# Kernel optimization log

Measured on AMD Instinct MI355X. Metric: run time of the kernel, lower is better.

## Reference

```python
import jax, jax.numpy as jnp
import numpy as np

D = 1024      # model dim
H = 16        # attention heads
E = 8         # experts
TOP_K = 2
CF = 1.25     # capacity factor
EPS = 1e-5
BAL_COEF = 1e-2
Z_COEF = 1e-3


def layer_norm(x, w, b):
    m = x.mean(-1, keepdims=True)
    var = ((x - m) ** 2).mean(-1, keepdims=True)
    return (x - m) * jax.lax.rsqrt(var + EPS) * w + b


def mha(q, k, v, in_w, in_b, out_w, out_b):
    B, S, d = q.shape
    dh = d // H
    wq, wk, wv = jnp.split(in_w, 3, axis=0)
    bq, bk, bv = jnp.split(in_b, 3)

    def proj(x, w, b):  # [B,S,d] -> [B,H,S,dh]
        return (x @ w.T + b).reshape(B, -1, H, dh).transpose(0, 2, 1, 3)

    qh, kh, vh = proj(q, wq, bq), proj(k, wk, bk), proj(v, wv, bv)
    scale = 1.0 / np.sqrt(dh)
    scores = jnp.einsum('bhqd,bhkd->bhqk', qh, kh) * scale
    attn = jax.nn.softmax(scores, axis=-1)
    o = jnp.einsum('bhqk,bhkd->bhqd', attn, vh).transpose(0, 2, 1, 3).reshape(B, S, d)
    return o @ out_w.T + out_b


def moe(x, router_w, w1, b1, w2, b2):
    B, S, d = x.shape
    t = x.reshape(-1, d)           # [N,d] tokens
    N = t.shape[0]
    C = int(np.ceil(TOP_K * N / E * CF))  # per-expert capacity (static)
    logits = t @ router_w          # [N,E]
    probs = jax.nn.softmax(logits, axis=-1)
    gates, idx = jax.lax.top_k(probs, TOP_K)   # [N,2]
    oh = jax.nn.one_hot(idx, E, dtype=t.dtype) # [N,2,E]
    m0, m1 = oh[:, 0], oh[:, 1]
    # position in expert buffer; first choices take priority over second
    pos0 = jnp.cumsum(m0, axis=0) - 1.0
    pos1 = jnp.cumsum(m1, axis=0) - 1.0 + m0.sum(axis=0, keepdims=True)
    v0 = m0 * (pos0 < C)
    v1 = m1 * (pos1 < C)
    p0 = jax.nn.one_hot(pos0.astype(jnp.int32), C, dtype=t.dtype) * v0[..., None]  # [N,E,C]
    p1 = jax.nn.one_hot(pos1.astype(jnp.int32), C, dtype=t.dtype) * v1[..., None]
    dispatch = p0 + p1
    combine = p0 * gates[:, 0, None, None] + p1 * gates[:, 1, None, None]
    # dispatch -> grouped GEMM -> combine
    xin = jnp.einsum('nec,nd->ecd', dispatch, t)                     # [E,C,d]
    h = jax.nn.gelu(jnp.einsum('ecd,edf->ecf', xin, w1) + b1[:, None, :])
    out_e = jnp.einsum('ecf,efd->ecd', h, w2) + b2[:, None, :]       # [E,C,d]
    y = jnp.einsum('nec,ecd->nd', combine, out_e).reshape(B, S, d)
    # aux losses: load-balance + router z-loss
    f = m0.mean(axis=0)            # fraction routed (top-1)
    P = probs.mean(axis=0)         # mean router prob
    balance = E * jnp.sum(f * P)
    zloss = jnp.mean(jax.nn.logsumexp(logits, axis=-1) ** 2)
    aux = BAL_COEF * balance + Z_COEF * zloss
    return y, aux


def setup_inputs() -> dict:
    key = jax.random.key(0)
    ks = jax.random.split(key, 16)
    s = 0.02
    Dff = 4 * D
    return {
        'q': jax.random.normal(ks[0], (8, 512, D), jnp.float32),
        'k': jax.random.normal(ks[1], (8, 512, D), jnp.float32),
        'v': jax.random.normal(ks[2], (8, 512, D), jnp.float32),
        'in_proj_w': jax.random.normal(ks[3], (3 * D, D), jnp.float32) * s,
        'in_proj_b': jnp.zeros((3 * D,), jnp.float32),
        'out_proj_w': jax.random.normal(ks[4], (D, D), jnp.float32) * s,
        'out_proj_b': jnp.zeros((D,), jnp.float32),
        'ln1_w': jnp.ones((D,), jnp.float32),
        'ln1_b': jnp.zeros((D,), jnp.float32),
        'ln2_w': jnp.ones((D,), jnp.float32),
        'ln2_b': jnp.zeros((D,), jnp.float32),
        'router_w': jax.random.normal(ks[5], (D, E), jnp.float32) * s,
        'w1': jax.random.normal(ks[6], (E, D, Dff), jnp.float32) * s,
        'b1': jnp.zeros((E, Dff), jnp.float32),
        'w2': jax.random.normal(ks[7], (E, Dff, D), jnp.float32) * s,
        'b2': jnp.zeros((E, D), jnp.float32),
    }


def reference(q, k, v, in_proj_w, in_proj_b, out_proj_w, out_proj_b,
              ln1_w, ln1_b, ln2_w, ln2_b, router_w, w1, b1, w2, b2):
    attn = mha(q, k, v, in_proj_w, in_proj_b, out_proj_w, out_proj_b)
    x = layer_norm(q + attn, ln1_w, ln1_b)
    y, aux = moe(x, router_w, w1, b1, w2, b2)
    x = layer_norm(x + y, ln2_w, ln2_b)
    return x, aux
```

## Files before the change

kernel.cpp:

```cpp
#include <hip/hip_runtime.h>
#include <cstdint>
#include <cstddef>

#define KB   8
#define KS   512
#define KD   1024
#define KH   16
#define KDH  64
#define KE   8
#define KDFF 4096
#define KN   4096
#define KCAP 1280
#define KCHB 32
#define KNCH 4

typedef unsigned short u16;
typedef _Float16 f16;
typedef f16   f16x8 __attribute__((ext_vector_type(8)));
typedef float f32x4 __attribute__((ext_vector_type(4)));

#define RSCALE 4096.0f
#define RINV   2.44140625e-4f

__device__ __forceinline__ u16 f2h(float f){
  f16 h = (f16)f;
  return __builtin_bit_cast(u16, h);
}
__device__ __forceinline__ float h2f(u16 u){
  f16 h = __builtin_bit_cast(f16, u);
  return (float)h;
}
__device__ __forceinline__ void split2v(float f, u16 &a, u16 &b){
  f16 h0 = (f16)f;
  float r = (f - (float)h0) * RSCALE;
  a = __builtin_bit_cast(u16, h0);
  b = f2h(r);
}
__device__ __forceinline__ f16x8 ld8h(const u16* p){
  uint4 v = *(const uint4*)p;
  return __builtin_bit_cast(f16x8, v);
}
__device__ __forceinline__ void async16(const u16* g, u16* l){
  __builtin_amdgcn_global_load_lds(
      (const __attribute__((address_space(1))) unsigned int*)(g),
      (__attribute__((address_space(3))) unsigned int*)(l),
      16, 0, 0);
}

struct GArgs {
  const u16 *A0, *A1;
  const u16 *B0, *B1;
  long lda, sA, ldb, sB;
  const float* bias; long biasStride;
  float* outF;
  u16 *o0;
  int K, mode;
  float scale;
};

template<int NP>
__launch_bounds__(256)
__global__ void gemm128(GArgs g){
  __shared__ __align__(16) u16 sm[NP*2*4096];
  const int tid  = threadIdx.x;
  const int lane = tid & 63;
  const int wave = tid >> 6;
  const int quad = lane >> 4;
  const int r    = lane & 15;
  const int wm = (wave & 1) * 64;
  const int wn = (wave >> 1) * 64;
  const int z  = blockIdx.z;
  const long m0 = (long)blockIdx.y * 128;
  const long n0 = (long)blockIdx.x * 128;
  const u16* Ap[NP]; const u16* Bp[NP];
  Ap[0] = g.A0 + (long)z*g.sA; Bp[0] = g.B0 + (long)z*g.sB;
  if (NP == 2){ Ap[1] = g.A1 + (long)z*g.sA; Bp[1] = g.B1 + (long)z*g.sB; }
  const int srow   = tid >> 2;
  const int schunk = (tid & 3) ^ ((tid >> 3) & 3);
  f32x4 acc[4][4] = {};
  f32x4 accr[4][4] = {};
  for (int kt = 0; kt < g.K; kt += 32){
#pragma unroll
    for (int p = 0; p < NP; ++p){
#pragma unroll
      for (int r0 = 0; r0 < 2; ++r0){
        long row = r0*64 + srow;
        async16(Ap[p] + (m0 + row)*g.lda + kt + schunk*8, &sm[p*4096      + r0*2048 + wave*512]);
        async16(Bp[p] + (n0 + row)*g.ldb + kt + schunk*8, &sm[(NP+p)*4096 + r0*2048 + wave*512]);
      }
    }
    __syncthreads();
    f16x8 af[NP][4], bf[NP][4];
#pragma unroll
    for (int i = 0; i < 4; ++i){
      int row = wm + i*16 + r;
      int slot = quad ^ ((row >> 1) & 3);
#pragma unroll
      for (int p = 0; p < NP; ++p)
        af[p][i] = ld8h(&sm[p*4096 + row*32 + slot*8]);
    }
#pragma unroll
    for (int j = 0; j < 4; ++j){
      int row = wn + j*16 + r;
      int slot = quad ^ ((row >> 1) & 3);
#pragma unroll
      for (int p = 0; p < NP; ++p)
        bf[p][j] = ld8h(&sm[(NP+p)*4096 + row*32 + slot*8]);
    }
#pragma unroll
    for (int i = 0; i < 4; ++i)
#pragma unroll
      for (int j = 0; j < 4; ++j){
        acc[i][j] = __builtin_amdgcn_mfma_f32_16x16x32_f16(af[0][i], bf[0][j], acc[i][j], 0, 0, 0);
        if (NP == 2){
          accr[i][j] = __builtin_amdgcn_mfma_f32_16x16x32_f16(af[0][i], bf[1][j], accr[i][j], 0, 0, 0);
          accr[i][j] = __builtin_amdgcn_mfma_f32_16x16x32_f16(af[1][i], bf[0][j], accr[i][j], 0, 0, 0);
        }
      }
    __syncthreads();
  }
#pragma unroll
  for (int i = 0; i < 4; ++i){
#pragma unroll
    for (int rr = 0; rr < 4; ++rr){
      long row = m0 + wm + i*16 + quad*4 + rr;
#pragma unroll
      for (int j = 0; j < 4; ++j){
        long col = n0 + wn + j*16 + r;
        float v = acc[i][j][rr];
        if (NP == 2) v += accr[i][j][rr] * RINV;
        switch (g.mode){
          case 2: {
            g.outF[((long)z*KS + row)*KS + col] = v * g.scale;
            break;
          }
          case 4: {
            v += g.bias[col];
            g.outF[row*KD + col] = v;
            break;
          }
          case 5: {
            v += g.bias[(long)z*g.biasStride + col];
            float u = v + 0.044715f*v*v*v;
            v = 0.5f*v*(1.0f + tanhf(0.7978845608028654f*u));
            g.o0[((long)z*KCAP + row)*KDFF + col] = f2h(v);
            break;
          }
          case 6: {
            v += g.bias[(long)z*g.biasStride + col];
            g.o0[((long)z*KCAP + row)*KD + col] = f2h(v);
            break;
          }
          default: {
            v += g.bias[(long)z*g.biasStride + col];
            long b = row >> 9, s = row & 511;
            long h = col >> 6, d = col & 63;
            long idx = (z < 2) ? (((b*KH + h)*KS + s)*KDH + d)
                               : (((b*KH + h)*KDH + d)*KS + s);
            u16* d0 = g.o0 + (long)z * 2 * ((long)KN*KD);
            u16* d1 = d0 + (long)KN*KD;
            unsigned short x, y; split2v(v, x, y);
            d0[idx] = x; d1[idx] = y;
            break;
          }
        }
      }
    }
  }
}

__launch_bounds__(256)
__global__ void gemm_pv(const u16* __restrict__ Ph, const u16* __restrict__ Pl,
                        const u16* __restrict__ V0, const u16* __restrict__ V1,
                        u16* __restrict__ O0, u16* __restrict__ O1, int chunkBase){
  __shared__ __align__(16) u16 sm[2*4096 + 2*2048];
  const int tid  = threadIdx.x;
  const int lane = tid & 63;
  const int wave = tid >> 6;
  const int quad = lane >> 4;
  const int r    = lane & 15;
  const int wm = (wave & 1) * 64;
  const int wn = (wave >> 1) * 32;
  const int z  = blockIdx.y;
  const long m0 = (long)blockIdx.x * 128;
  const u16* Ap[2] = { Ph + (long)z*KS*KS,  Pl + (long)z*KS*KS };
  const u16* Bp[2] = { V0 + (long)z*KDH*KS, V1 + (long)z*KDH*KS };
  const int srow   = tid >> 2;
  const int schunk = (tid & 3) ^ ((tid >> 3) & 3);
  f32x4 acc[4][2] = {};
  f32x4 accr[4][2] = {};
  for (int kt = 0; kt < KS; kt += 32){
#pragma unroll
    for (int p = 0; p < 2; ++p){
#pragma unroll
      for (int r0 = 0; r0 < 2; ++r0){
        long row = r0*64 + srow;
        async16(Ap[p] + (m0 + row)*KS + kt + schunk*8, &sm[p*4096 + r0*2048 + wave*512]);
      }
      async16(Bp[p] + srow*KS + kt + schunk*8, &sm[8192 + p*2048 + wave*512]);
    }
    __syncthreads();
    f16x8 af[2][4], bf[2][2];
#pragma unroll
    for (int i = 0; i < 4; ++i){
      int row = wm + i*16 + r;
      int slot = quad ^ ((row >> 1) & 3);
#pragma unroll
      for (int p = 0; p < 2; ++p)
        af[p][i] = ld8h(&sm[p*4096 + row*32 + slot*8]);
    }
#pragma unroll
    for (int j = 0; j < 2; ++j){
      int row = wn + j*16 + r;
      int slot = quad ^ ((row >> 1) & 3);
#pragma unroll
      for (int p = 0; p < 2; ++p)
        bf[p][j] = ld8h(&sm[8192 + p*2048 + row*32 + slot*8]);
    }
#pragma unroll
    for (int i = 0; i < 4; ++i)
#pragma unroll
      for (int j = 0; j < 2; ++j){
        acc[i][j]  = __builtin_amdgcn_mfma_f32_16x16x32_f16(af[0][i], bf[0][j], acc[i][j], 0, 0, 0);
        accr[i][j] = __builtin_amdgcn_mfma_f32_16x16x32_f16(af[0][i], bf[1][j], accr[i][j], 0, 0, 0);
        accr[i][j] = __builtin_amdgcn_mfma_f32_16x16x32_f16(af[1][i], bf[0][j], accr[i][j], 0, 0, 0);
      }
    __syncthreads();
  }
  int bh = chunkBase + z;
  long b = bh >> 4, h = bh & 15;
#pragma unroll
  for (int i = 0; i < 4; ++i){
#pragma unroll
    for (int rr = 0; rr < 4; ++rr){
      long s = m0 + wm + i*16 + quad*4 + rr;
#pragma unroll
      for (int j = 0; j < 2; ++j){
        long col = wn + j*16 + r;
        float v = acc[i][j][rr] + accr[i][j][rr] * RINV;
        long idx = (b*KS + s)*KD + h*KDH + col;
        unsigned short x, y; split2v(v, x, y);
        O0[idx] = x; O1[idx] = y;
      }
    }
  }
}

__global__ void split2k(const float* __restrict__ x, u16* __restrict__ h,
                        u16* __restrict__ l, long n4){
  long i = (long)blockIdx.x*blockDim.x + threadIdx.x;
  if (i >= n4) return;
  float4 v = ((const float4*)x)[i];
  ushort4 a, b;
  split2v(v.x, a.x, b.x);
  split2v(v.y, a.y, b.y);
  split2v(v.z, a.z, b.z);
  split2v(v.w, a.w, b.w);
  ((ushort4*)h)[i] = a; ((ushort4*)l)[i] = b;
}

__global__ void trans_b(const float* __restrict__ in, u16* __restrict__ outp, int R, int Cc){
  __shared__ float tile[32][33];
  long z = blockIdx.z;
  const float* ip = in + z*(long)R*Cc;
  u16* op = outp + z*(long)R*Cc;
  int c0 = blockIdx.x*32, r0 = blockIdx.y*32;
  int tx = threadIdx.x, ty = threadIdx.y;
  for (int rr = ty; rr < 32; rr += 8)
    tile[rr][tx] = ip[(long)(r0+rr)*Cc + c0 + tx];
  __syncthreads();
  for (int cc = ty; cc < 32; cc += 8)
    op[(long)(c0+cc)*R + r0 + tx] = f2h(tile[tx][cc]);
}

__launch_bounds__(64)
__global__ void softmax2(const float* __restrict__ scores, u16* __restrict__ ph,
                         u16* __restrict__ pl){
  long row = blockIdx.x;
  const float* rp = scores + row * KS;
  int lane = threadIdx.x;
  float4 a = ((const float4*)rp)[lane*2];
  float4 b = ((const float4*)rp)[lane*2 + 1];
  float vv[8] = {a.x,a.y,a.z,a.w,b.x,b.y,b.z,b.w};
  float m = vv[0];
#pragma unroll
  for (int t = 1; t < 8; ++t) m = fmaxf(m, vv[t]);
  for (int off = 32; off; off >>= 1) m = fmaxf(m, __shfl_xor(m, off));
  float s = 0.f;
#pragma unroll
  for (int t = 0; t < 8; ++t){ vv[t] = expf(vv[t] - m); s += vv[t]; }
  for (int off = 32; off; off >>= 1) s += __shfl_xor(s, off);
  float inv = 1.0f / s;
  unsigned short hh[8], ll[8];
#pragma unroll
  for (int t = 0; t < 8; ++t) split2v(vv[t] * inv, hh[t], ll[t]);
  ushort4* dh = (ushort4*)(ph + row*KS + lane*8);
  dh[0] = make_ushort4(hh[0],hh[1],hh[2],hh[3]);
  dh[1] = make_ushort4(hh[4],hh[5],hh[6],hh[7]);
  ushort4* dl = (ushort4*)(pl + row*KS + lane*8);
  dl[0] = make_ushort4(ll[0],ll[1],ll[2],ll[3]);
  dl[1] = make_ushort4(ll[4],ll[5],ll[6],ll[7]);
}

__launch_bounds__(256)
__global__ void ln1_router(const float* __restrict__ q, const float* __restrict__ attn,
    const float* __restrict__ lnw, const float* __restrict__ lnb, const float* __restrict__ rw,
    float* __restrict__ x1, u16* __restrict__ x1b,
    int* __restrict__ idx0, int* __restrict__ idx1, float* __restrict__ gate0, float* __restrict__ gate1,
    float* __restrict__ ptok, float* __restrict__ lset){
  const int t = blockIdx.x, tid = threadIdx.x;
  const int lane = tid & 63, wid = tid >> 6;
  float4 xv = ((const float4*)(q    + (long)t*KD))[tid];
  float4 av = ((const float4*)(attn + (long)t*KD))[tid];
  xv.x += av.x; xv.y += av.y; xv.z += av.z; xv.w += av.w;
  float s  = xv.x + xv.y + xv.z + xv.w;
  float ss = xv.x*xv.x + xv.y*xv.y + xv.z*xv.z + xv.w*xv.w;
  for (int off = 32; off; off >>= 1){ s += __shfl_xor(s, off); ss += __shfl_xor(ss, off); }
  __shared__ float rs[4], rss[4];
  if (lane == 0){ rs[wid] = s; rss[wid] = ss; }
  __syncthreads();
  float S1 = rs[0]+rs[1]+rs[2]+rs[3];
  float S2 = rss[0]+rss[1]+rss[2]+rss[3];
  float mean = S1 * (1.0f/KD);
  float var  = S2 * (1.0f/KD) - mean*mean;
  float rstd = rsqrtf(var + 1e-5f);
  float4 w4 = ((const float4*)lnw)[tid];
  float4 b4 = ((const float4*)lnb)[tid];
  float y0 = (xv.x - mean)*rstd*w4.x + b4.x;
  float y1 = (xv.y - mean)*rstd*w4.y + b4.y;
  float y2 = (xv.z - mean)*rstd*w4.z + b4.z;
  float y3 = (xv.w - mean)*rstd*w4.w + b4.w;
  float4 yo; yo.x=y0; yo.y=y1; yo.z=y2; yo.w=y3;
  ((float4*)(x1 + (long)t*KD))[tid] = yo;
  ushort4 yb; yb.x=f2h(y0); yb.y=f2h(y1); yb.z=f2h(y2); yb.w=f2h(y3);
  ((ushort4*)(x1b + (long)t*KD))[tid] = yb;
  int d0 = tid*4;
  float rloc[4][8];
#pragma unroll
  for (int c = 0; c < 4; ++c){
    const float4* rp = (const float4*)(rw + (long)(d0 + c)*KE);
    float4 u = rp[0], v2 = rp[1];
    rloc[c][0]=u.x; rloc[c][1]=u.y; rloc[c][2]=u.z; rloc[c][3]=u.w;
    rloc[c][4]=v2.x; rloc[c][5]=v2.y; rloc[c][6]=v2.z; rloc[c][7]=v2.w;
  }
  float yv[4] = {y0,y1,y2,y3};
  float pr[8];
#pragma unroll
  for (int e = 0; e < 8; ++e)
    pr[e] = yv[0]*rloc[0][e] + yv[1]*rloc[1][e] + yv[2]*rloc[2][e] + yv[3]*rloc[3][e];
#pragma unroll
  for (int e = 0; e < 8; ++e)
    for (int off = 32; off; off >>= 1) pr[e] += __shfl_xor(pr[e], off);
  __shared__ float wl[4][8];
  if (lane == 0)
#pragma unroll
    for (int e = 0; e < 8; ++e) wl[wid][e] = pr[e];
  __syncthreads();
  if (tid == 0){
    float lg[8];
#pragma unroll
    for (int e = 0; e < 8; ++e) lg[e] = wl[0][e]+wl[1][e]+wl[2][e]+wl[3][e];
    float mx = lg[0];
    for (int e = 1; e < 8; ++e) mx = fmaxf(mx, lg[e]);
    float pe[8], se = 0.f;
    for (int e = 0; e < 8; ++e){ pe[e] = expf(lg[e]-mx); se += pe[e]; }
    float inv = 1.0f/se;
    for (int e = 0; e < 8; ++e) pe[e] *= inv;
    int e0 = 0;
    for (int e = 1; e < 8; ++e) if (pe[e] > pe[e0]) e0 = e;
    int e1 = (e0 == 0) ? 1 : 0;
    for (int e = 0; e < 8; ++e) if (e != e0 && pe[e] > pe[e1]) e1 = e;
    idx0[t] = e0; idx1[t] = e1;
    gate0[t] = pe[e0]; gate1[t] = pe[e1];
    for (int e = 0; e < 8; ++e) ptok[(long)t*8 + e] = pe[e];
    lset[t] = mx + logf(se);
  }
}

__launch_bounds__(64)
__global__ void scan1(const int* __restrict__ idx0, const int* __restrict__ idx1,
                      int* __restrict__ rnk0, int* __restrict__ rnk1,
                      int* __restrict__ h0, int* __restrict__ h1){
  int lane = threadIdx.x;
  int t = blockIdx.x*64 + lane;
  int i0 = idx0[t], i1 = idx1[t];
  unsigned long long below = (1ull << lane) - 1ull;
  unsigned long long b0[8], b1[8];
#pragma unroll
  for (int e = 0; e < 8; ++e){
    b0[e] = __ballot(i0 == e);
    b1[e] = __ballot(i1 == e);
  }
  rnk0[t] = __popcll(b0[i0] & below);
  rnk1[t] = __popcll(b1[i1] & below);
  if (lane < 8){
    h0[blockIdx.x*8 + lane] = __popcll(b0[lane]);
    h1[blockIdx.x*8 + lane] = __popcll(b1[lane]);
  }
}

__launch_bounds__(64)
__global__ void scan2(const int* __restrict__ h0, const int* __restrict__ h1,
                      int* __restrict__ bs0, int* __restrict__ bs1, int* __restrict__ cnt0){
  int lane = threadIdx.x;
  for (int e = 0; e < 8; ++e){
    int v = h0[lane*8 + e];
    int x = v;
    for (int off = 1; off < 64; off <<= 1){
      int y = __shfl_up(x, off);
      if (lane >= off) x += y;
    }
    bs0[lane*8 + e] = x - v;
    int tot = __shfl(x, 63);
    if (lane == 0) cnt0[e] = tot;
    int w = h1[lane*8 + e];
    int xx = w;
    for (int off = 1; off < 64; off <<= 1){
      int y = __shfl_up(xx, off);
      if (lane >= off) xx += y;
    }
    bs1[lane*8 + e] = tot + xx - w;
  }
}

__global__ void scan3(const int* __restrict__ idx0, const int* __restrict__ idx1,
                      const int* __restrict__ rnk0, const int* __restrict__ rnk1,
                      const int* __restrict__ bs0, const int* __restrict__ bs1,
                      int* __restrict__ dst0, int* __restrict__ dst1, int* __restrict__ slot){
  int t = blockIdx.x*blockDim.x + threadIdx.x;
  if (t >= KN) return;
  int c = t >> 6;
  int e0 = idx0[t], e1 = idx1[t];
  int p0 = bs0[c*8 + e0] + rnk0[t];
  int p1 = bs1[c*8 + e1] + rnk1[t];
  int d0 = (p0 < KCAP) ? (e0*KCAP + p0) : -1;
  int d1 = (p1 < KCAP) ? (e1*KCAP + p1) : -1;
  dst0[t] = d0; dst1[t] = d1;
  if (d0 >= 0) slot[d0] = t;
  if (d1 >= 0) slot[d1] = t;
}

__launch_bounds__(64)
__global__ void gather_xin(const int* __restrict__ slot_token, const u16* __restrict__ x1b,
                           u16* __restrict__ xin){
  long slot = blockIdx.x;
  int t = slot_token[slot];
  uint4* dst = (uint4*)(xin + slot*KD);
  int lane = threadIdx.x;
  if (t >= 0){
    const uint4* src = (const uint4*)(x1b + (long)t*KD);
    dst[lane*2]   = src[lane*2];
    dst[lane*2+1] = src[lane*2+1];
  } else {
    uint4 zz; zz.x = zz.y = zz.z = zz.w = 0;
    dst[lane*2] = zz; dst[lane*2+1] = zz;
  }
}

__launch_bounds__(256)
__global__ void combine_ln2(const float* __restrict__ x1, const u16* __restrict__ oute,
    const int* __restrict__ dest0, const int* __restrict__ dest1,
    const float* __restrict__ gate0, const float* __restrict__ gate1,
    const float* __restrict__ lnw, const float* __restrict__ lnb, float* __restrict__ out){
  const int t = blockIdx.x, tid = threadIdx.x;
  const int lane = tid & 63, wid = tid >> 6;
  float4 xv = ((const float4*)(x1 + (long)t*KD))[tid];
  int d0 = dest0[t], d1 = dest1[t];
  float g0 = gate0[t], g1 = gate1[t];
  if (d0 >= 0){
    ushort4 o = ((const ushort4*)(oute + (long)d0*KD))[tid];
    xv.x += g0*h2f(o.x); xv.y += g0*h2f(o.y); xv.z += g0*h2f(o.z); xv.w += g0*h2f(o.w);
  }
  if (d1 >= 0){
    ushort4 o = ((const ushort4*)(oute + (long)d1*KD))[tid];
    xv.x += g1*h2f(o.x); xv.y += g1*h2f(o.y); xv.z += g1*h2f(o.z); xv.w += g1*h2f(o.w);
  }
  float s  = xv.x + xv.y + xv.z + xv.w;
  float ss = xv.x*xv.x + xv.y*xv.y + xv.z*xv.z + xv.w*xv.w;
  for (int off = 32; off; off >>= 1){ s += __shfl_xor(s, off); ss += __shfl_xor(ss, off); }
  __shared__ float rs[4], rss[4];
  if (lane == 0){ rs[wid] = s; rss[wid] = ss; }
  __syncthreads();
  float S1 = rs[0]+rs[1]+rs[2]+rs[3];
  float S2 = rss[0]+rss[1]+rss[2]+rss[3];
  float mean = S1 * (1.0f/KD);
  float var  = S2 * (1.0f/KD) - mean*mean;
  float rstd = rsqrtf(var + 1e-5f);
  float4 w4 = ((const float4*)lnw)[tid];
  float4 b4 = ((const float4*)lnb)[tid];
  float4 yo;
  yo.x = (xv.x - mean)*rstd*w4.x + b4.x;
  yo.y = (xv.y - mean)*rstd*w4.y + b4.y;
  yo.z = (xv.z - mean)*rstd*w4.z + b4.z;
  yo.w = (xv.w - mean)*rstd*w4.w + b4.w;
  ((float4*)(out + (long)t*KD))[tid] = yo;
}

__launch_bounds__(1024)
__global__ void aux_k(const int* __restrict__ cnt0, const float* __restrict__ ptok,
                      const float* __restrict__ lset, float* __restrict__ out){
  int t = threadIdx.x;
  float ps[8] = {0,0,0,0,0,0,0,0};
  float l2 = 0.f;
  for (int i = t; i < KN; i += 1024){
    const float4* p = (const float4*)(ptok + (long)i*8);
    float4 a = p[0], b = p[1];
    ps[0]+=a.x; ps[1]+=a.y; ps[2]+=a.z; ps[3]+=a.w;
    ps[4]+=b.x; ps[5]+=b.y; ps[6]+=b.z; ps[7]+=b.w;
    float l = lset[i]; l2 = fmaf(l, l, l2);
  }
#pragma unroll
  for (int off = 32; off; off >>= 1){
#pragma unroll
    for (int e = 0; e < 8; ++e) ps[e] += __shfl_xor(ps[e], off);
    l2 += __shfl_xor(l2, off);
  }
  __shared__ float sp[16][9];
  int lane = t & 63, wid = t >> 6;
  if (lane == 0){
#pragma unroll
    for (int e = 0; e < 8; ++e) sp[wid][e] = ps[e];
    sp[wid][8] = l2;
  }
  __syncthreads();
  if (t == 0){
    float fin[9];
#pragma unroll
    for (int j = 0; j < 9; ++j){
      float s = 0.f;
      for (int w2 = 0; w2 < 16; ++w2) s += sp[w2][j];
      fin[j] = s;
    }
    float bal = 0.f;
    for (int e = 0; e < 8; ++e)
      bal += ((float)cnt0[e] * (1.0f/KN)) * (fin[e] * (1.0f/KN));
    bal *= (float)KE;
    float zl = fin[8] * (1.0f/KN);
    out[(long)KN*KD] = 0.01f*bal + 0.001f*zl;
  }
}

extern "C" void kernel_launch(void* const* d_in, const int* in_sizes, int n_in,
                              void* d_out, int out_size, void* d_ws, size_t ws_size,
                              hipStream_t stream){
  const float* q    = (const float*)d_in[0];
  const float* k    = (const float*)d_in[1];
  const float* v    = (const float*)d_in[2];
  const float* inw  = (const float*)d_in[3];
  const float* inb  = (const float*)d_in[4];
  const float* outw = (const float*)d_in[5];
  const float* outb = (const float*)d_in[6];
  const float* ln1w = (const float*)d_in[7];
  const float* ln1b = (const float*)d_in[8];
  const float* ln2w = (const float*)d_in[9];
  const float* ln2b = (const float*)d_in[10];
  const float* rw   = (const float*)d_in[11];
  const float* w1   = (const float*)d_in[12];
  const float* b1   = (const float*)d_in[13];
  const float* w2   = (const float*)d_in[14];
  const float* b2   = (const float*)d_in[15];
  float* out = (float*)d_out;
  char* ws = (char*)d_ws;

  constexpr size_t PLB  = (size_t)KN*KD*2;
  constexpr long   PLE  = (long)KN*KD;
  constexpr size_t oW1T = 0;
  constexpr size_t oW2T = oW1T + 67108864;
  constexpr size_t oWQ0 = oW2T + 67108864;
  constexpr size_t oWQ1 = oWQ0 + 6291456;
  constexpr size_t oWO0 = oWQ1 + 6291456;
  constexpr size_t oWO1 = oWO0 + 2097152;
  constexpr size_t oX1  = oWO1 + 2097152;
  constexpr size_t oX1B = oX1  + 16777216;
  constexpr size_t oMISC= oX1B + 8388608;
  constexpr size_t oU1  = oMISC + 1048576;
  constexpr size_t oU2  = oU1 + 83886080;
  constexpr size_t oU3  = oU2 + 50331648;
  constexpr size_t oEND = oU3 + 67108864;
  if (ws_size < oEND) return;

  u16* W1T = (u16*)(ws + oW1T);
  u16* W2T = (u16*)(ws + oW2T);
  u16* WQ0 = (u16*)(ws + oWQ0); u16* WQ1 = (u16*)(ws + oWQ1);
  u16* WO0 = (u16*)(ws + oWO0); u16* WO1 = (u16*)(ws + oWO1);
  float* X1 = (float*)(ws + oX1);
  u16* X1B  = (u16*)(ws + oX1B);

  int*   IDX0 = (int*)(ws + oMISC);
  int*   IDX1 = (int*)(ws + oMISC + 16384);
  int*   RNK0 = (int*)(ws + oMISC + 32768);
  int*   RNK1 = (int*)(ws + oMISC + 49152);
  int*   DST0 = (int*)(ws + oMISC + 65536);
  int*   DST1 = (int*)(ws + oMISC + 81920);
  float* G0   = (float*)(ws + oMISC + 98304);
  float* G1   = (float*)(ws + oMISC + 114688);
  int*   H0   = (int*)(ws + oMISC + 131072);
  int*   H1   = (int*)(ws + oMISC + 133120);
  int*   BS0  = (int*)(ws + oMISC + 135168);
  int*   BS1  = (int*)(ws + oMISC + 137216);
  int*   CNT0 = (int*)(ws + oMISC + 139264);
  int*   SLOT = (int*)(ws + oMISC + 139776);
  float* PTOK = (float*)(ws + oMISC + 262144);
  float* LSET = (float*)(ws + oMISC + 393216);

  u16* Qs0 = (u16*)(ws + oU1);           u16* Qs1 = (u16*)(ws + oU1 + PLB);
  u16* Ks0 = (u16*)(ws + oU1 + 2*PLB);   u16* Ks1 = (u16*)(ws + oU1 + 3*PLB);
  u16* Vs0 = (u16*)(ws + oU1 + 4*PLB);   u16* Vs1 = (u16*)(ws + oU1 + 5*PLB);
  float* ATTN = (float*)(ws + oU1);
  u16* O0 = (u16*)(ws + oU1 + 16777216);
  u16* O1 = (u16*)(ws + oU1 + 16777216 + PLB);
  u16* HBUF = (u16*)(ws + oU1);

  u16* QH0 = (u16*)(ws + oU2);           u16* QH1 = (u16*)(ws + oU2 + PLB);
  u16* KH0 = (u16*)(ws + oU2 + 2*PLB);   u16* KH1 = (u16*)(ws + oU2 + 3*PLB);
  u16* VT0 = (u16*)(ws + oU2 + 4*PLB);   u16* VT1 = (u16*)(ws + oU2 + 5*PLB);
  u16* XIN  = (u16*)(ws + oU2);
  u16* OUTE = (u16*)(ws + oU2 + 20971520);

  float* SCF = (float*)(ws + oU3);
  u16* PH  = (u16*)(ws + oU3 + 33554432);
  u16* PL  = (u16*)(ws + oU3 + 50331648);

  hipMemsetAsync(ws + oMISC + 139776, 0xFF, (size_t)KE*KCAP*4, stream);

  split2k<<<4096, 256, 0, stream>>>(q, Qs0, Qs1, (long)KN*KD/4);
  split2k<<<4096, 256, 0, stream>>>(k, Ks0, Ks1, (long)KN*KD/4);
  split2k<<<4096, 256, 0, stream>>>(v, Vs0, Vs1, (long)KN*KD/4);
  split2k<<<3072, 256, 0, stream>>>(inw, WQ0, WQ1, 786432);
  split2k<<<1024, 256, 0, stream>>>(outw, WO0, WO1, 262144);

  trans_b<<<dim3(KDFF/32, KD/32, KE), dim3(32,8), 0, stream>>>(w1, W1T, KD, KDFF);
  trans_b<<<dim3(KD/32, KDFF/32, KE), dim3(32,8), 0, stream>>>(w2, W2T, KDFF, KD);

  {
    GArgs ga{};
    ga.A0=Qs0; ga.A1=Qs1; ga.lda=KD; ga.sA=2*PLE;
    ga.B0=WQ0; ga.B1=WQ1; ga.ldb=KD; ga.sB=1048576;
    ga.bias=inb; ga.biasStride=KD;
    ga.o0=QH0; ga.outF=nullptr;
    ga.K=KD; ga.mode=7; ga.scale=1.f;
    gemm128<2><<<dim3(8, 32, 3), 256, 0, stream>>>(ga);
  }

  for (int c = 0; c < KNCH; ++c){
    long hoff = (long)c * KCHB * KS * KDH;
    GArgs gs{};
    gs.A0=QH0+hoff; gs.A1=QH1+hoff; gs.lda=KDH; gs.sA=(long)KS*KDH;
    gs.B0=KH0+hoff; gs.B1=KH1+hoff; gs.ldb=KDH; gs.sB=(long)KS*KDH;
    gs.bias=nullptr; gs.biasStride=0; gs.outF=SCF; gs.o0=nullptr;
    gs.K=KDH; gs.mode=2; gs.scale=0.125f;
    gemm128<2><<<dim3(4, 4, KCHB), 256, 0, stream>>>(gs);

    softmax2<<<KCHB*KS, 64, 0, stream>>>(SCF, PH, PL);

    gemm_pv<<<dim3(4, KCHB), 256, 0, stream>>>(PH, PL, VT0+hoff, VT1+hoff,
                                               O0, O1, c*KCHB);
  }

  {
    GArgs go{};
    go.A0=O0; go.A1=O1; go.lda=KD; go.sA=0;
    go.B0=WO0; go.B1=WO1; go.ldb=KD; go.sB=0;
    go.bias=outb; go.biasStride=0; go.outF=ATTN; go.o0=nullptr;
    go.K=KD; go.mode=4; go.scale=1.f;
    gemm128<2><<<dim3(8, 32, 1), 256, 0, stream>>>(go);
  }

  ln1_router<<<KN, 256, 0, stream>>>(q, ATTN, ln1w, ln1b, rw, X1, X1B,
                                     IDX0, IDX1, G0, G1, PTOK, LSET);
  scan1<<<64, 64, 0, stream>>>(IDX0, IDX1, RNK0, RNK1, H0, H1);
  scan2<<<1, 64, 0, stream>>>(H0, H1, BS0, BS1, CNT0);
  scan3<<<16, 256, 0, stream>>>(IDX0, IDX1, RNK0, RNK1, BS0, BS1, DST0, DST1, SLOT);
  aux_k<<<1, 1024, 0, stream>>>(CNT0, PTOK, LSET, out);
  gather_xin<<<KE*KCAP, 64, 0, stream>>>(SLOT, X1B, XIN);

  {
    GArgs f1{};
    f1.A0=XIN; f1.A1=nullptr; f1.lda=KD; f1.sA=(long)KCAP*KD;
    f1.B0=W1T; f1.B1=nullptr; f1.ldb=KD; f1.sB=(long)KDFF*KD;
    f1.bias=b1; f1.biasStride=KDFF; f1.outF=nullptr; f1.o0=HBUF;
    f1.K=KD; f1.mode=5; f1.scale=1.f;
    gemm128<1><<<dim3(KDFF/128, KCAP/128, KE), 256, 0, stream>>>(f1);

    GArgs f2{};
    f2.A0=HBUF; f2.A1=nullptr; f2.lda=KDFF; f2.sA=(long)KCAP*KDFF;
    f2.B0=W2T; f2.B1=nullptr; f2.ldb=KDFF; f2.sB=(long)KD*KDFF;
    f2.bias=b2; f2.biasStride=KD; f2.outF=nullptr; f2.o0=OUTE;
    f2.K=KDFF; f2.mode=6; f2.scale=1.f;
    gemm128<1><<<dim3(KD/128, KCAP/128, KE), 256, 0, stream>>>(f2);
  }

  combine_ln2<<<KN, 256, 0, stream>>>(X1, OUTE, DST0, DST1, G0, G1, ln2w, ln2b, out);
}
```

Measured before the change: 1.351 ms.

## Write QKV projections token-major, transpose V separately, remap workgroups across XCDs

The QKV projection epilogue now writes Q and K in token-major [N,D] layout with coalesced stores instead of scattering into head-major layout. The QK^T GEMM indexes heads directly through a row stride of KD, and V gets a separate tiled transpose kernel to build its [B,H,dh,S] layout. Both GEMM kernels also remap linear workgroup IDs so that consecutive tiles land on the same XCD, aiming for better L2 reuse. The cost is an extra kernel launch and an extra pass over V.

```diff
diff --git a/kernel.cpp b/kernel.cpp
--- a/kernel.cpp
+++ b/kernel.cpp
@@ -13,6 +13,7 @@
 #define KCAP 1280
 #define KCHB 32
 #define KNCH 4
+#define KPLE ((long)KN*KD)
 
 typedef unsigned short u16;
 typedef _Float16 f16;
@@ -45,6 +46,12 @@
       (const __attribute__((address_space(1))) unsigned int*)(g),
       (__attribute__((address_space(3))) unsigned int*)(l),
       16, 0, 0);
+}
+
+__device__ __forceinline__ int xcd_remap(int lin, int nwg){
+  int qq = nwg >> 3, r8 = nwg & 7;
+  int xcd = lin & 7, pos = lin >> 3;
+  return (xcd < r8 ? xcd*(qq+1) : r8*(qq+1) + (xcd-r8)*qq) + pos;
 }
 
 struct GArgs {
@@ -54,7 +61,9 @@
   const float* bias; long biasStride;
   float* outF;
   u16 *o0;
+  u16 *o1;
   int K, mode;
+  int hbase;
   float scale;
 };
 
@@ -69,12 +78,25 @@
   const int r    = lane & 15;
   const int wm = (wave & 1) * 64;
   const int wn = (wave >> 1) * 64;
-  const int z  = blockIdx.z;
-  const long m0 = (long)blockIdx.y * 128;
-  const long n0 = (long)blockIdx.x * 128;
+  const int gx = gridDim.x, gy = gridDim.y;
+  const int nwg = gx*gy*(int)gridDim.z;
+  int lin = (int)blockIdx.x + gx*((int)blockIdx.y + gy*(int)blockIdx.z);
+  lin = xcd_remap(lin, nwg);
+  const int bx = lin % gx;
+  const int byy = (lin / gx) % gy;
+  const int z  = lin / (gx*gy);
+  const long m0 = (long)byy * 128;
+  const long n0 = (long)bx * 128;
   const u16* Ap[NP]; const u16* Bp[NP];
-  Ap[0] = g.A0 + (long)z*g.sA; Bp[0] = g.B0 + (long)z*g.sB;
-  if (NP == 2){ Ap[1] = g.A1 + (long)z*g.sA; Bp[1] = g.B1 + (long)z*g.sB; }
+  if (g.mode == 2){
+    int bh = g.hbase + z;
+    long off = ((long)(bh >> 4)*KS)*KD + (long)(bh & 15)*KDH;
+    Ap[0] = g.A0 + off; Bp[0] = g.B0 + off;
+    if (NP == 2){ Ap[1] = g.A1 + off; Bp[1] = g.B1 + off; }
+  } else {
+    Ap[0] = g.A0 + (long)z*g.sA; Bp[0] = g.B0 + (long)z*g.sB;
+    if (NP == 2){ Ap[1] = g.A1 + (long)z*g.sA; Bp[1] = g.B1 + (long)z*g.sB; }
+  }
   const int srow   = tid >> 2;
   const int schunk = (tid & 3) ^ ((tid >> 3) & 3);
   f32x4 acc[4][4] = {};
@@ -153,12 +175,9 @@
           }
           default: {
             v += g.bias[(long)z*g.biasStride + col];
-            long b = row >> 9, s = row & 511;
-            long h = col >> 6, d = col & 63;
-            long idx = (z < 2) ? (((b*KH + h)*KS + s)*KDH + d)
-                               : (((b*KH + h)*KDH + d)*KS + s);
-            u16* d0 = g.o0 + (long)z * 2 * ((long)KN*KD);
-            u16* d1 = d0 + (long)KN*KD;
+            u16* d0 = (z < 2) ? (g.o0 + (long)z*2*KPLE) : g.o1;
+            u16* d1 = d0 + KPLE;
+            long idx = row*KD + col;
             unsigned short x, y; split2v(v, x, y);
             d0[idx] = x; d1[idx] = y;
             break;
@@ -181,8 +200,12 @@
   const int r    = lane & 15;
   const int wm = (wave & 1) * 64;
   const int wn = (wave >> 1) * 32;
-  const int z  = blockIdx.y;
-  const long m0 = (long)blockIdx.x * 128;
+  const int gx = gridDim.x;
+  const int nwg = gx*(int)gridDim.y;
+  int lin = (int)blockIdx.x + gx*(int)blockIdx.y;
+  lin = xcd_remap(lin, nwg);
+  const int z  = lin / gx;
+  const long m0 = (long)(lin % gx) * 128;
   const u16* Ap[2] = { Ph + (long)z*KS*KS,  Pl + (long)z*KS*KS };
   const u16* Bp[2] = { V0 + (long)z*KDH*KS, V1 + (long)z*KDH*KS };
   const int srow   = tid >> 2;
@@ -271,6 +294,31 @@
   __syncthreads();
   for (int cc = ty; cc < 32; cc += 8)
     op[(long)(c0+cc)*R + r0 + tx] = f2h(tile[tx][cc]);
+}
+
+__global__ void vtrans(const u16* __restrict__ in0, const u16* __restrict__ in1,
+                       u16* __restrict__ out0, u16* __restrict__ out1){
+  __shared__ u16 tile[2][32][33];
+  int sT = blockIdx.x;
+  int dT = blockIdx.y;
+  int b  = blockIdx.z;
+  int tx = threadIdx.x;
+  int ty = threadIdx.y;
+  long srow = (long)b*KS + sT*32;
+  int d0 = dT*32;
+  for (int rr = ty; rr < 32; rr += 8){
+    tile[0][rr][tx] = in0[(srow+rr)*KD + d0 + tx];
+    tile[1][rr][tx] = in1[(srow+rr)*KD + d0 + tx];
+  }
+  __syncthreads();
+  int h = d0 >> 6;
+  int dbase = d0 & 63;
+  long obase = ((long)(b*KH + h)*KDH)*KS + sT*32 + tx;
+  for (int cc = ty; cc < 32; cc += 8){
+    long o = obase + (long)(dbase+cc)*KS;
+    out0[o] = tile[0][tx][cc];
+    out1[o] = tile[1][tx][cc];
+  }
 }
 
 __launch_bounds__(64)
@@ -606,13 +654,14 @@
   u16* Qs0 = (u16*)(ws + oU1);           u16* Qs1 = (u16*)(ws + oU1 + PLB);
   u16* Ks0 = (u16*)(ws + oU1 + 2*PLB);   u16* Ks1 = (u16*)(ws + oU1 + 3*PLB);
   u16* Vs0 = (u16*)(ws + oU1 + 4*PLB);   u16* Vs1 = (u16*)(ws + oU1 + 5*PLB);
+  u16* VTOK0 = (u16*)(ws + oU1 + 6*PLB); u16* VTOK1 = (u16*)(ws + oU1 + 7*PLB);
   float* ATTN = (float*)(ws + oU1);
   u16* O0 = (u16*)(ws + oU1 + 16777216);
   u16* O1 = (u16*)(ws + oU1 + 16777216 + PLB);
   u16* HBUF = (u16*)(ws + oU1);
 
-  u16* QH0 = (u16*)(ws + oU2);           u16* QH1 = (u16*)(ws + oU2 + PLB);
-  u16* KH0 = (u16*)(ws + oU2 + 2*PLB);   u16* KH1 = (u16*)(ws + oU2 + 3*PLB);
+  u16* QT0 = (u16*)(ws + oU2);           u16* QT1 = (u16*)(ws + oU2 + PLB);
+  u16* KT0 = (u16*)(ws + oU2 + 2*PLB);   u16* KT1 = (u16*)(ws + oU2 + 3*PLB);
   u16* VT0 = (u16*)(ws + oU2 + 4*PLB);   u16* VT1 = (u16*)(ws + oU2 + 5*PLB);
   u16* XIN  = (u16*)(ws + oU2);
   u16* OUTE = (u16*)(ws + oU2 + 20971520);
@@ -637,16 +686,19 @@
     ga.A0=Qs0; ga.A1=Qs1; ga.lda=KD; ga.sA=2*PLE;
     ga.B0=WQ0; ga.B1=WQ1; ga.ldb=KD; ga.sB=1048576;
     ga.bias=inb; ga.biasStride=KD;
-    ga.o0=QH0; ga.outF=nullptr;
+    ga.o0=QT0; ga.o1=VTOK0; ga.outF=nullptr;
     ga.K=KD; ga.mode=7; ga.scale=1.f;
     gemm128<2><<<dim3(8, 32, 3), 256, 0, stream>>>(ga);
   }
+
+  vtrans<<<dim3(KS/32, KD/32, KB), dim3(32,8), 0, stream>>>(VTOK0, VTOK1, VT0, VT1);
 
   for (int c = 0; c < KNCH; ++c){
     long hoff = (long)c * KCHB * KS * KDH;
     GArgs gs{};
-    gs.A0=QH0+hoff; gs.A1=QH1+hoff; gs.lda=KDH; gs.sA=(long)KS*KDH;
-    gs.B0=KH0+hoff; gs.B1=KH1+hoff; gs.ldb=KDH; gs.sB=(long)KS*KDH;
+    gs.A0=QT0; gs.A1=QT1; gs.lda=KD; gs.sA=0;
+    gs.B0=KT0; gs.B1=KT1; gs.ldb=KD; gs.sB=0;
+    gs.hbase = c*KCHB;
     gs.bias=nullptr; gs.biasStride=0; gs.outF=SCF; gs.o0=nullptr;
     gs.K=KDH; gs.mode=2; gs.scale=0.125f;
     gemm128<2><<<dim3(4, 4, KCHB), 256, 0, stream>>>(gs);
```

After: 1.279 ms. 5.4% less time.
